# Kernel optimization log

Measured on AMD Instinct MI355X. Metric: run time of the kernel, lower is better.

## Reference

```python
import jax, jax.numpy as jnp
import numpy as np
import math

B, R, S, CE, H, C = 1, 384, 2048, 64, 8, 8
INF = 1e9
EPS = 1e-10


def setup_inputs() -> dict:
    key = jax.random.key(0)
    ks = jax.random.split(key, 10)
    m = jax.random.normal(ks[0], (B, R, S, CE), jnp.float32)
    mask = (jax.random.uniform(ks[1], (B, R, S)) > 0.1).astype(jnp.float32)
    glorot = lambda k, shp: (jax.random.normal(k, shp, jnp.float32)
                             * math.sqrt(2.0 / (shp[0] + shp[1])))
    Wq = glorot(ks[2], (H * C, CE))
    Wk = glorot(ks[3], (C, CE))
    Wv = glorot(ks[4], (C, CE))
    Wg = glorot(ks[5], (H * C, CE))
    bg = jnp.zeros((H * C,), jnp.float32)
    Wo = glorot(ks[6], (CE, H * C))
    bo = jnp.zeros((CE,), jnp.float32)
    add_to = jax.random.normal(ks[7], (B, S, R, CE), jnp.float32)
    return {"m": m, "mask": mask, "Wq": Wq, "Wk": Wk, "Wv": Wv,
            "Wg": Wg, "bg": bg, "Wo": Wo, "bo": bo, "add_to": add_to}


def reference(m, mask, Wq, Wk, Wv, Wg, bg, Wo, bo, add_to):
    # masked mean-pooled query over the extra-seq axis: [b, R, CE]
    q_num = jnp.sum(m * mask[..., None], axis=-2)
    q_den = jnp.sum(mask, axis=-1) + EPS
    q = q_num / q_den[..., None]
    # project + scale + split heads: [b, R, H, C]
    q = (q @ Wq.T) * math.sqrt(1.0 / C)
    q = q.reshape(q.shape[:-1] + (H, C))
    k = m @ Wk.T  # [b, R, S, C]
    v = m @ Wv.T  # [b, R, S, C]
    # attention logits [b, R, H, S] with mask bias then softmax over S
    a = jnp.einsum("brhc,brsc->brhs", q, k)
    bias = ((mask - 1.0) * INF)[..., None, :]  # [b, R, 1, S]
    a = jax.nn.softmax(a + bias, axis=-1)
    o = jnp.einsum("brhs,brsc->brhc", a, v)  # [b, R, H, C]
    # sigmoid gate per position: [b, R, S, H, C]
    g = jax.nn.sigmoid(m @ Wg.T + bg)
    g = g.reshape(g.shape[:-1] + (H, C))
    o = o[..., None, :, :] * g  # broadcast over S
    o = o.reshape(o.shape[:-2] + (H * C,))  # [b, R, S, H*C]
    # output projection, transpose (R<->S), fused residual add
    out = add_to + jnp.swapaxes(o @ Wo.T + bo, -2, -3)  # [b, S, R, CE]
    return out
```

## Files before the change

kernel.cpp:

```cpp
#include <hip/hip_runtime.h>

#define SS 2048
#define RR 384
#define CED 64

typedef __attribute__((ext_vector_type(8))) short bf16x8;
typedef __attribute__((ext_vector_type(4))) float f32x4;

__device__ __forceinline__ short f2bf(float f) {
  union { float f; unsigned u; } v; v.f = f;
  unsigned u = v.u;
  u += 0x7fffu + ((u >> 16) & 1u);
  return (short)(u >> 16);
}
__device__ __forceinline__ float bf2f(short s) {
  union { unsigned u; float f; } v;
  v.u = ((unsigned)(unsigned short)s) << 16;
  return v.f;
}

__global__ __launch_bounds__(256) void kW(const float* __restrict__ Wk,
                                          const float* __restrict__ Wv,
                                          const float* __restrict__ Wg,
                                          const float* __restrict__ Wo,
                                          short* __restrict__ wkv,
                                          short* __restrict__ wgb,
                                          short* __restrict__ wob) {
  int t = blockIdx.x * 256 + threadIdx.x;
  if (t < 1024) {
    int c16 = t >> 6, ce = t & 63;
    float v = (c16 < 8) ? Wk[c16 * 64 + ce] : Wv[(c16 - 8) * 64 + ce];
    wkv[t] = f2bf(v);
  }
  if (t < 4096) {
    wgb[t] = f2bf(Wg[t]);
    wob[t] = f2bf(Wo[t]);
  }
}

__global__ __launch_bounds__(256) void kA(const float* __restrict__ m,
                                          const float* __restrict__ mask,
                                          const float* __restrict__ Wq,
                                          const short* __restrict__ wkv,
                                          float* __restrict__ o_ws) {
  __shared__ __align__(16) short kv[SS][16];
  __shared__ __align__(16) float qs[64];
  __shared__ __align__(16) float qpart[4][64];
  __shared__ float redmax[4][8];
  __shared__ float redsum[4][8];
  __shared__ float ored[4][64];
  __shared__ float qden_l[4];

  const int r = blockIdx.x;
  const int tid = threadIdx.x;
  const int wave = tid >> 6, lane = tid & 63;
  const int l15 = lane & 15, quad = lane >> 4;

  bf16x8 bkv0 = *(const bf16x8*)(wkv + l15 * 64 + quad * 8);
  bf16x8 bkv1 = *(const bf16x8*)(wkv + l15 * 64 + 32 + quad * 8);

  float qdp = 0.f;
  float pp[16];
#pragma unroll
  for (int i = 0; i < 16; i++) pp[i] = 0.f;

  for (int s0 = wave * 16; s0 < SS; s0 += 64) {
    const int row = s0 + l15;
    const float* mrow = m + ((size_t)r * SS + row) * CED;
    f32x4 a0 = *(const f32x4*)(mrow + quad * 8);
    f32x4 a1 = *(const f32x4*)(mrow + quad * 8 + 4);
    f32x4 a2 = *(const f32x4*)(mrow + 32 + quad * 8);
    f32x4 a3 = *(const f32x4*)(mrow + 32 + quad * 8 + 4);
    float mk = mask[r * SS + row];
    qdp += mk;

    pp[0] += a0.x * mk;  pp[1] += a0.y * mk;  pp[2] += a0.z * mk;  pp[3] += a0.w * mk;
    pp[4] += a1.x * mk;  pp[5] += a1.y * mk;  pp[6] += a1.z * mk;  pp[7] += a1.w * mk;
    pp[8] += a2.x * mk;  pp[9] += a2.y * mk;  pp[10] += a2.z * mk; pp[11] += a2.w * mk;
    pp[12] += a3.x * mk; pp[13] += a3.y * mk; pp[14] += a3.z * mk; pp[15] += a3.w * mk;

    bf16x8 af0 = {f2bf(a0.x), f2bf(a0.y), f2bf(a0.z), f2bf(a0.w),
                  f2bf(a1.x), f2bf(a1.y), f2bf(a1.z), f2bf(a1.w)};
    bf16x8 af1 = {f2bf(a2.x), f2bf(a2.y), f2bf(a2.z), f2bf(a2.w),
                  f2bf(a3.x), f2bf(a3.y), f2bf(a3.z), f2bf(a3.w)};
    f32x4 acc = {0.f, 0.f, 0.f, 0.f};
    acc = __builtin_amdgcn_mfma_f32_16x16x32_bf16(af0, bkv0, acc, 0, 0, 0);
    acc = __builtin_amdgcn_mfma_f32_16x16x32_bf16(af1, bkv1, acc, 0, 0, 0);
#pragma unroll
    for (int rg = 0; rg < 4; rg++)
      kv[s0 + quad * 4 + rg][l15] = f2bf(acc[rg]);
  }

#pragma unroll
  for (int d = 1; d < 16; d <<= 1) {
#pragma unroll
    for (int i = 0; i < 16; i++) pp[i] += __shfl_xor(pp[i], d);
  }
#pragma unroll
  for (int d = 1; d < 16; d <<= 1) qdp += __shfl_xor(qdp, d);
  if (l15 == 0) {
#pragma unroll
    for (int i = 0; i < 8; i++) {
      qpart[wave][quad * 8 + i] = pp[i];
      qpart[wave][32 + quad * 8 + i] = pp[8 + i];
    }
  }
  if (lane == 0) qden_l[wave] = qdp;
  __syncthreads();

  if (wave == 0) {
    float qden = qden_l[0] + qden_l[1] + qden_l[2] + qden_l[3] + 1e-10f;
    float inv = 1.f / qden;
    const float* wqrow = Wq + lane * CED;
    float acc = 0.f;
    for (int ce = 0; ce < CED; ce++) {
      float qv = qpart[0][ce] + qpart[1][ce] + qpart[2][ce] + qpart[3][ce];
      acc += qv * wqrow[ce];
    }
    qs[lane] = acc * inv * 0.35355339059327373f;
  }
  __syncthreads();

  float q[64];
#pragma unroll
  for (int i = 0; i < 16; i++) ((f32x4*)q)[i] = ((const f32x4*)qs)[i];

  float lg[8][8];
  float mx[8];
#pragma unroll
  for (int h = 0; h < 8; h++) mx[h] = -3.0e38f;

#pragma unroll
  for (int j = 0; j < 8; j++) {
    int s = tid + 256 * j;
    bf16x8 k8 = *(const bf16x8*)&kv[s][0];
    float kf[8];
#pragma unroll
    for (int c = 0; c < 8; c++) kf[c] = bf2f(k8[c]);
    float bias = (mask[r * SS + s] - 1.f) * 1e9f;
#pragma unroll
    for (int h = 0; h < 8; h++) {
      float a = bias;
#pragma unroll
      for (int c = 0; c < 8; c++) a += q[h * 8 + c] * kf[c];
      lg[j][h] = a;
      mx[h] = fmaxf(mx[h], a);
    }
  }
#pragma unroll
  for (int d = 1; d < 64; d <<= 1) {
#pragma unroll
    for (int h = 0; h < 8; h++) mx[h] = fmaxf(mx[h], __shfl_xor(mx[h], d));
  }
  if (lane == 0) {
#pragma unroll
    for (int h = 0; h < 8; h++) redmax[wave][h] = mx[h];
  }
  __syncthreads();
  float Mh[8];
#pragma unroll
  for (int h = 0; h < 8; h++)
    Mh[h] = fmaxf(fmaxf(redmax[0][h], redmax[1][h]),
                  fmaxf(redmax[2][h], redmax[3][h]));

  float sm[8] = {0, 0, 0, 0, 0, 0, 0, 0};
#pragma unroll
  for (int j = 0; j < 8; j++) {
    int s = tid + 256 * j;
#pragma unroll
    for (int h = 0; h < 8; h++) {
      float p = __expf(lg[j][h] - Mh[h]);
      sm[h] += p;
      kv[s][h] = f2bf(p);
    }
  }
#pragma unroll
  for (int d = 1; d < 64; d <<= 1) {
#pragma unroll
    for (int h = 0; h < 8; h++) sm[h] += __shfl_xor(sm[h], d);
  }
  if (lane == 0) {
#pragma unroll
    for (int h = 0; h < 8; h++) redsum[wave][h] = sm[h];
  }
  __syncthreads();

  {
    int h = (tid >> 3) & 7, c = tid & 7, q4 = tid >> 6;
    float a0 = 0, a1 = 0, a2 = 0, a3 = 0;
    int sbeg = q4 * 512;
    for (int s = sbeg; s < sbeg + 512; s += 4) {
      a0 += bf2f(kv[s][h]) * bf2f(kv[s][8 + c]);
      a1 += bf2f(kv[s + 1][h]) * bf2f(kv[s + 1][8 + c]);
      a2 += bf2f(kv[s + 2][h]) * bf2f(kv[s + 2][8 + c]);
      a3 += bf2f(kv[s + 3][h]) * bf2f(kv[s + 3][8 + c]);
    }
    ored[q4][tid & 63] = (a0 + a1) + (a2 + a3);
  }
  __syncthreads();
  if (tid < 64) {
    int h = tid >> 3;
    float ssum = redsum[0][h] + redsum[1][h] + redsum[2][h] + redsum[3][h];
    float o = ored[0][tid] + ored[1][tid] + ored[2][tid] + ored[3][tid];
    o_ws[r * 64 + tid] = o / ssum;
  }
}

__global__ __launch_bounds__(256) void kB(const float* __restrict__ m,
                                          const float* __restrict__ add_to,
                                          const float* __restrict__ bg,
                                          const float* __restrict__ bo,
                                          const float* __restrict__ o_ws,
                                          const short* __restrict__ wg,
                                          const short* __restrict__ wo,
                                          float* __restrict__ out) {
  __shared__ __align__(16) short Tl[64][72];
  __shared__ __align__(16) float Yl[64][68];

  const int bx = blockIdx.x;
  const int sg = bx / 384;
  const int r = bx - sg * 384;
  const int s0 = sg * 64;
  const int tid = threadIdx.x;
  const int wave = tid >> 6, lane = tid & 63;
  const int l15 = lane & 15, quad = lane >> 4;

  const int row = s0 + wave * 16 + l15;
  const float* mrow = m + ((size_t)r * SS + row) * CED;
  f32x4 x0 = *(const f32x4*)(mrow + quad * 8);
  f32x4 x1 = *(const f32x4*)(mrow + quad * 8 + 4);
  f32x4 x2 = *(const f32x4*)(mrow + 32 + quad * 8);
  f32x4 x3 = *(const f32x4*)(mrow + 32 + quad * 8 + 4);

  bf16x8 wgf[4][2], wof[4][2];
#pragma unroll
  for (int nt = 0; nt < 4; nt++) {
#pragma unroll
    for (int kc = 0; kc < 2; kc++) {
      wgf[nt][kc] = *(const bf16x8*)(wg + (nt * 16 + l15) * 64 + kc * 32 + quad * 8);
      wof[nt][kc] = *(const bf16x8*)(wo + (nt * 16 + l15) * 64 + kc * 32 + quad * 8);
    }
  }

  const int sp = tid >> 2, cb = (tid & 3) * 16;
  const float* ap = add_to + ((size_t)(s0 + sp) * RR + r) * CED + cb;
  f32x4 at0 = ((const f32x4*)ap)[0];
  f32x4 at1 = ((const f32x4*)ap)[1];
  f32x4 at2 = ((const f32x4*)ap)[2];
  f32x4 at3 = ((const f32x4*)ap)[3];

  float ov[4];
#pragma unroll
  for (int nt = 0; nt < 4; nt++) ov[nt] = o_ws[r * 64 + nt * 16 + l15];

  f32x4 acc[4] = {{0,0,0,0},{0,0,0,0},{0,0,0,0},{0,0,0,0}};
  {
    bf16x8 af0 = {f2bf(x0.x), f2bf(x0.y), f2bf(x0.z), f2bf(x0.w),
                  f2bf(x1.x), f2bf(x1.y), f2bf(x1.z), f2bf(x1.w)};
    bf16x8 af1 = {f2bf(x2.x), f2bf(x2.y), f2bf(x2.z), f2bf(x2.w),
                  f2bf(x3.x), f2bf(x3.y), f2bf(x3.z), f2bf(x3.w)};
#pragma unroll
    for (int nt = 0; nt < 4; nt++) {
      acc[nt] = __builtin_amdgcn_mfma_f32_16x16x32_bf16(af0, wgf[nt][0], acc[nt], 0, 0, 0);
      acc[nt] = __builtin_amdgcn_mfma_f32_16x16x32_bf16(af1, wgf[nt][1], acc[nt], 0, 0, 0);
    }
  }
#pragma unroll
  for (int nt = 0; nt < 4; nt++) {
    float bgv = bg[nt * 16 + l15];
#pragma unroll
    for (int rg = 0; rg < 4; rg++) {
      float val = acc[nt][rg] + bgv;
      float gt = 1.f / (1.f + __expf(-val));
      Tl[wave * 16 + quad * 4 + rg][nt * 16 + l15] = f2bf(gt * ov[nt]);
    }
  }
  __syncthreads();

  f32x4 acc2[4] = {{0,0,0,0},{0,0,0,0},{0,0,0,0},{0,0,0,0}};
#pragma unroll
  for (int kc = 0; kc < 2; kc++) {
    bf16x8 af = *(const bf16x8*)&Tl[wave * 16 + l15][kc * 32 + quad * 8];
#pragma unroll
    for (int nt = 0; nt < 4; nt++)
      acc2[nt] = __builtin_amdgcn_mfma_f32_16x16x32_bf16(af, wof[nt][kc], acc2[nt], 0, 0, 0);
  }
#pragma unroll
  for (int nt = 0; nt < 4; nt++) {
#pragma unroll
    for (int rg = 0; rg < 4; rg++)
      Yl[wave * 16 + quad * 4 + rg][nt * 16 + l15] = acc2[nt][rg];
  }
  __syncthreads();

  float* op = out + ((size_t)(s0 + sp) * RR + r) * CED + cb;
  f32x4 y0 = *(const f32x4*)&Yl[sp][cb];
  f32x4 y1 = *(const f32x4*)&Yl[sp][cb + 4];
  f32x4 y2 = *(const f32x4*)&Yl[sp][cb + 8];
  f32x4 y3 = *(const f32x4*)&Yl[sp][cb + 12];
  f32x4 b0 = *(const f32x4*)(bo + cb);
  f32x4 b1 = *(const f32x4*)(bo + cb + 4);
  f32x4 b2 = *(const f32x4*)(bo + cb + 8);
  f32x4 b3 = *(const f32x4*)(bo + cb + 12);
  ((f32x4*)op)[0] = at0 + y0 + b0;
  ((f32x4*)op)[1] = at1 + y1 + b1;
  ((f32x4*)op)[2] = at2 + y2 + b2;
  ((f32x4*)op)[3] = at3 + y3 + b3;
}

extern "C" void kernel_launch(void* const* d_in, const int* in_sizes, int n_in,
                              void* d_out, int out_size, void* d_ws, size_t ws_size,
                              hipStream_t stream) {
  const float* m      = (const float*)d_in[0];
  const float* mask   = (const float*)d_in[1];
  const float* Wq     = (const float*)d_in[2];
  const float* Wk     = (const float*)d_in[3];
  const float* Wv     = (const float*)d_in[4];
  const float* Wg     = (const float*)d_in[5];
  const float* bg     = (const float*)d_in[6];
  const float* Wo     = (const float*)d_in[7];
  const float* bo     = (const float*)d_in[8];
  const float* add_to = (const float*)d_in[9];
  float* out = (float*)d_out;

  char* ws = (char*)d_ws;
  float* o_ws = (float*)ws;
  short* wkv  = (short*)(ws + 98304);
  short* wgb  = (short*)(ws + 98304 + 2048);
  short* wob  = (short*)(ws + 98304 + 2048 + 8192);

  hipLaunchKernelGGL(kW, dim3(16),    dim3(256), 0, stream, Wk, Wv, Wg, Wo, wkv, wgb, wob);
  hipLaunchKernelGGL(kA, dim3(384),   dim3(256), 0, stream, m, mask, Wq, wkv, o_ws);
  hipLaunchKernelGGL(kB, dim3(12288), dim3(256), 0, stream, m, add_to, bg, bo, o_ws, wgb, wob, out);
}
```

Baseline: 588.8 us.

## Restructure gate/output kernel to tile over R per S with fully contiguous output stores

The gate/output-projection kernel now launches one block per S position and loops over six 64-row R tiles, instead of one block per (S-tile, r). Each tile writes a contiguous 64x64 chunk of the transposed output, and add_to is read contiguously too. The m reads become strided, since each row comes from a different r. The next tile's m rows are prefetched into registers, and weights and biases are loaded once per block. In exchange the grid is smaller, there are serial loop iterations with two barriers each, and m gathers are less coalesced.

```diff
diff --git a/kernel.cpp b/kernel.cpp
--- a/kernel.cpp
+++ b/kernel.cpp
@@ -217,20 +217,11 @@
   __shared__ __align__(16) short Tl[64][72];
   __shared__ __align__(16) float Yl[64][68];
 
-  const int bx = blockIdx.x;
-  const int sg = bx / 384;
-  const int r = bx - sg * 384;
-  const int s0 = sg * 64;
+  const int s = blockIdx.x;
   const int tid = threadIdx.x;
   const int wave = tid >> 6, lane = tid & 63;
   const int l15 = lane & 15, quad = lane >> 4;
-
-  const int row = s0 + wave * 16 + l15;
-  const float* mrow = m + ((size_t)r * SS + row) * CED;
-  f32x4 x0 = *(const f32x4*)(mrow + quad * 8);
-  f32x4 x1 = *(const f32x4*)(mrow + quad * 8 + 4);
-  f32x4 x2 = *(const f32x4*)(mrow + 32 + quad * 8);
-  f32x4 x3 = *(const f32x4*)(mrow + 32 + quad * 8 + 4);
+  const int sp = tid >> 2, cb = (tid & 3) * 16;
 
   bf16x8 wgf[4][2], wof[4][2];
 #pragma unroll
@@ -241,71 +232,104 @@
       wof[nt][kc] = *(const bf16x8*)(wo + (nt * 16 + l15) * 64 + kc * 32 + quad * 8);
     }
   }
-
-  const int sp = tid >> 2, cb = (tid & 3) * 16;
-  const float* ap = add_to + ((size_t)(s0 + sp) * RR + r) * CED + cb;
-  f32x4 at0 = ((const f32x4*)ap)[0];
-  f32x4 at1 = ((const f32x4*)ap)[1];
-  f32x4 at2 = ((const f32x4*)ap)[2];
-  f32x4 at3 = ((const f32x4*)ap)[3];
-
-  float ov[4];
-#pragma unroll
-  for (int nt = 0; nt < 4; nt++) ov[nt] = o_ws[r * 64 + nt * 16 + l15];
-
-  f32x4 acc[4] = {{0,0,0,0},{0,0,0,0},{0,0,0,0},{0,0,0,0}};
+  float bgv[4];
+#pragma unroll
+  for (int nt = 0; nt < 4; nt++) bgv[nt] = bg[nt * 16 + l15];
+  f32x4 bov[4];
+#pragma unroll
+  for (int i = 0; i < 4; i++) bov[i] = *(const f32x4*)(bo + cb + i * 4);
+
+  f32x4 mc[4];
   {
-    bf16x8 af0 = {f2bf(x0.x), f2bf(x0.y), f2bf(x0.z), f2bf(x0.w),
-                  f2bf(x1.x), f2bf(x1.y), f2bf(x1.z), f2bf(x1.w)};
-    bf16x8 af1 = {f2bf(x2.x), f2bf(x2.y), f2bf(x2.z), f2bf(x2.w),
-                  f2bf(x3.x), f2bf(x3.y), f2bf(x3.z), f2bf(x3.w)};
+    const float* mp = m + ((size_t)(wave * 16 + l15) * SS + s) * CED;
+    mc[0] = *(const f32x4*)(mp + quad * 8);
+    mc[1] = *(const f32x4*)(mp + quad * 8 + 4);
+    mc[2] = *(const f32x4*)(mp + 32 + quad * 8);
+    mc[3] = *(const f32x4*)(mp + 32 + quad * 8 + 4);
+  }
+
+#pragma unroll
+  for (int rt = 0; rt < 6; rt++) {
+    const int r0 = rt * 64;
+
+    f32x4 mn[4];
+    if (rt < 5) {
+      const float* mp = m + ((size_t)(r0 + 64 + wave * 16 + l15) * SS + s) * CED;
+      mn[0] = *(const f32x4*)(mp + quad * 8);
+      mn[1] = *(const f32x4*)(mp + quad * 8 + 4);
+      mn[2] = *(const f32x4*)(mp + 32 + quad * 8);
+      mn[3] = *(const f32x4*)(mp + 32 + quad * 8 + 4);
+    }
+
+    const float* ap = add_to + ((size_t)s * RR + r0 + sp) * CED + cb;
+    f32x4 at0 = ((const f32x4*)ap)[0];
+    f32x4 at1 = ((const f32x4*)ap)[1];
+    f32x4 at2 = ((const f32x4*)ap)[2];
+    f32x4 at3 = ((const f32x4*)ap)[3];
+
+    float o16[4][4];
+    {
+      const float* ob = o_ws + (r0 + wave * 16 + quad * 4) * 64 + l15;
+#pragma unroll
+      for (int rg = 0; rg < 4; rg++)
+#pragma unroll
+        for (int nt = 0; nt < 4; nt++)
+          o16[rg][nt] = ob[rg * 64 + nt * 16];
+    }
+
+    f32x4 acc[4] = {{0,0,0,0},{0,0,0,0},{0,0,0,0},{0,0,0,0}};
+    {
+      bf16x8 af0 = {f2bf(mc[0].x), f2bf(mc[0].y), f2bf(mc[0].z), f2bf(mc[0].w),
+                    f2bf(mc[1].x), f2bf(mc[1].y), f2bf(mc[1].z), f2bf(mc[1].w)};
+      bf16x8 af1 = {f2bf(mc[2].x), f2bf(mc[2].y), f2bf(mc[2].z), f2bf(mc[2].w),
+                    f2bf(mc[3].x), f2bf(mc[3].y), f2bf(mc[3].z), f2bf(mc[3].w)};
+#pragma unroll
+      for (int nt = 0; nt < 4; nt++) {
+        acc[nt] = __builtin_amdgcn_mfma_f32_16x16x32_bf16(af0, wgf[nt][0], acc[nt], 0, 0, 0);
+        acc[nt] = __builtin_amdgcn_mfma_f32_16x16x32_bf16(af1, wgf[nt][1], acc[nt], 0, 0, 0);
+      }
+    }
 #pragma unroll
     for (int nt = 0; nt < 4; nt++) {
-      acc[nt] = __builtin_amdgcn_mfma_f32_16x16x32_bf16(af0, wgf[nt][0], acc[nt], 0, 0, 0);
-      acc[nt] = __builtin_amdgcn_mfma_f32_16x16x32_bf16(af1, wgf[nt][1], acc[nt], 0, 0, 0);
-    }
-  }
-#pragma unroll
-  for (int nt = 0; nt < 4; nt++) {
-    float bgv = bg[nt * 16 + l15];
-#pragma unroll
-    for (int rg = 0; rg < 4; rg++) {
-      float val = acc[nt][rg] + bgv;
-      float gt = 1.f / (1.f + __expf(-val));
-      Tl[wave * 16 + quad * 4 + rg][nt * 16 + l15] = f2bf(gt * ov[nt]);
-    }
-  }
-  __syncthreads();
-
-  f32x4 acc2[4] = {{0,0,0,0},{0,0,0,0},{0,0,0,0},{0,0,0,0}};
-#pragma unroll
-  for (int kc = 0; kc < 2; kc++) {
-    bf16x8 af = *(const bf16x8*)&Tl[wave * 16 + l15][kc * 32 + quad * 8];
-#pragma unroll
-    for (int nt = 0; nt < 4; nt++)
-      acc2[nt] = __builtin_amdgcn_mfma_f32_16x16x32_bf16(af, wof[nt][kc], acc2[nt], 0, 0, 0);
-  }
-#pragma unroll
-  for (int nt = 0; nt < 4; nt++) {
-#pragma unroll
-    for (int rg = 0; rg < 4; rg++)
-      Yl[wave * 16 + quad * 4 + rg][nt * 16 + l15] = acc2[nt][rg];
-  }
-  __syncthreads();
-
-  float* op = out + ((size_t)(s0 + sp) * RR + r) * CED + cb;
-  f32x4 y0 = *(const f32x4*)&Yl[sp][cb];
-  f32x4 y1 = *(const f32x4*)&Yl[sp][cb + 4];
-  f32x4 y2 = *(const f32x4*)&Yl[sp][cb + 8];
-  f32x4 y3 = *(const f32x4*)&Yl[sp][cb + 12];
-  f32x4 b0 = *(const f32x4*)(bo + cb);
-  f32x4 b1 = *(const f32x4*)(bo + cb + 4);
-  f32x4 b2 = *(const f32x4*)(bo + cb + 8);
-  f32x4 b3 = *(const f32x4*)(bo + cb + 12);
-  ((f32x4*)op)[0] = at0 + y0 + b0;
-  ((f32x4*)op)[1] = at1 + y1 + b1;
-  ((f32x4*)op)[2] = at2 + y2 + b2;
-  ((f32x4*)op)[3] = at3 + y3 + b3;
+#pragma unroll
+      for (int rg = 0; rg < 4; rg++) {
+        float val = acc[nt][rg] + bgv[nt];
+        float gt = 1.f / (1.f + __expf(-val));
+        Tl[wave * 16 + quad * 4 + rg][nt * 16 + l15] = f2bf(gt * o16[rg][nt]);
+      }
+    }
+    __syncthreads();
+
+    f32x4 acc2[4] = {{0,0,0,0},{0,0,0,0},{0,0,0,0},{0,0,0,0}};
+#pragma unroll
+    for (int kc = 0; kc < 2; kc++) {
+      bf16x8 af = *(const bf16x8*)&Tl[wave * 16 + l15][kc * 32 + quad * 8];
+#pragma unroll
+      for (int nt = 0; nt < 4; nt++)
+        acc2[nt] = __builtin_amdgcn_mfma_f32_16x16x32_bf16(af, wof[nt][kc], acc2[nt], 0, 0, 0);
+    }
+#pragma unroll
+    for (int nt = 0; nt < 4; nt++) {
+#pragma unroll
+      for (int rg = 0; rg < 4; rg++)
+        Yl[wave * 16 + quad * 4 + rg][nt * 16 + l15] = acc2[nt][rg];
+    }
+    __syncthreads();
+
+    float* op = out + ((size_t)s * RR + r0 + sp) * CED + cb;
+    f32x4 y0 = *(const f32x4*)&Yl[sp][cb];
+    f32x4 y1 = *(const f32x4*)&Yl[sp][cb + 4];
+    f32x4 y2 = *(const f32x4*)&Yl[sp][cb + 8];
+    f32x4 y3 = *(const f32x4*)&Yl[sp][cb + 12];
+    ((f32x4*)op)[0] = at0 + y0 + bov[0];
+    ((f32x4*)op)[1] = at1 + y1 + bov[1];
+    ((f32x4*)op)[2] = at2 + y2 + bov[2];
+    ((f32x4*)op)[3] = at3 + y3 + bov[3];
+
+    if (rt < 5) {
+      mc[0] = mn[0]; mc[1] = mn[1]; mc[2] = mn[2]; mc[3] = mn[3];
+    }
+  }
 }
 
 extern "C" void kernel_launch(void* const* d_in, const int* in_sizes, int n_in,
@@ -329,7 +353,7 @@
   short* wgb  = (short*)(ws + 98304 + 2048);
   short* wob  = (short*)(ws + 98304 + 2048 + 8192);
 
-  hipLaunchKernelGGL(kW, dim3(16),    dim3(256), 0, stream, Wk, Wv, Wg, Wo, wkv, wgb, wob);
-  hipLaunchKernelGGL(kA, dim3(384),   dim3(256), 0, stream, m, mask, Wq, wkv, o_ws);
-  hipLaunchKernelGGL(kB, dim3(12288), dim3(256), 0, stream, m, add_to, bg, bo, o_ws, wgb, wob, out);
-}
+  hipLaunchKernelGGL(kW, dim3(16),   dim3(256), 0, stream, Wk, Wv, Wg, Wo, wkv, wgb, wob);
+  hipLaunchKernelGGL(kA, dim3(384),  dim3(256), 0, stream, m, mask, Wq, wkv, o_ws);
+  hipLaunchKernelGGL(kB, dim3(2048), dim3(256), 0, stream, m, add_to, bg, bo, o_ws, wgb, wob, out);
+}
```

After: 554.2 us. 1.06x faster.
